# Optimization experiments

Hardware: AMD Instinct MI355X
Metric: run time of the kernel (lower is better)

## Reference

```python
import jax, jax.numpy as jnp
import numpy as np

B, S, D_MODEL = 2, 2048, 2048
N_HEADS, N_KV_HEADS, D_HEAD = 32, 8, 64
INIT_STD = 0.02


def setup_inputs() -> dict:
    key = jax.random.key(0)
    k1, k2, k3, k4, k5 = jax.random.split(key, 5)
    return {
        "residual": jax.random.normal(k1, (B, S, D_MODEL), dtype=jnp.float32),
        "W_Q": jax.random.normal(k2, (N_HEADS, D_HEAD, D_MODEL), dtype=jnp.float32) * INIT_STD,
        "W_K": jax.random.normal(k3, (N_KV_HEADS, D_HEAD, D_MODEL), dtype=jnp.float32) * INIT_STD,
        "W_V": jax.random.normal(k4, (N_KV_HEADS, D_HEAD, D_MODEL), dtype=jnp.float32) * INIT_STD,
        "W_O": jax.random.normal(k5, (N_HEADS, D_HEAD, D_MODEL), dtype=jnp.float32) * INIT_STD,
    }


def reference(residual, W_Q, W_K, W_V, W_O):
    # QKV projections: residual [b,p,d] x W [n,h,d] -> [b,p,n,h]
    q = jnp.einsum('bpd,nhd->bpnh', residual, W_Q)
    k = jnp.einsum('bpd,nhd->bpnh', residual, W_K)
    v = jnp.einsum('bpd,nhd->bpnh', residual, W_V)

    # GQA: repeat_interleave kv heads up to n_heads
    rep = N_HEADS // N_KV_HEADS
    k = jnp.repeat(k, rep, axis=2)  # [b, p, n_heads, h]
    v = jnp.repeat(v, rep, axis=2)

    # scaled dot-product scores: [b, n, q, k]
    scores = jnp.einsum('bqnh,bknh->bnqk', q, k) / jnp.sqrt(jnp.float32(D_HEAD))

    # causal mask (seq_len == total_len, no cache)
    seq_len = residual.shape[1]
    causal = jnp.tril(jnp.ones((seq_len, seq_len), dtype=bool))
    scores = jnp.where(causal[None, None, :, :], scores, jnp.float32(-jnp.inf))

    pattern = jax.nn.softmax(scores, axis=-1)

    # weighted sum of values: [b, q, n, h]
    attn_out = jnp.einsum('bnqk,bknh->bqnh', pattern, v)

    # output projection: [b, q, d_model]
    out = jnp.einsum('bqnh,nhd->bqd', attn_out, W_O)
    return out
```

## Files before the change

kernel.cpp:

```cpp
#include <hip/hip_runtime.h>


typedef __attribute__((ext_vector_type(8))) short short8;
typedef __attribute__((ext_vector_type(4))) short short4v;
typedef __attribute__((ext_vector_type(4))) float f32x4;

__device__ __forceinline__ short f2bs(float f) {
  unsigned u = __float_as_uint(f);
  u = (u + 0x7fffu + ((u >> 16) & 1u)) >> 16;
  return (short)u;
}
__device__ __forceinline__ float bs2f(short s) {
  return __uint_as_float(((unsigned)(unsigned short)s) << 16);
}

__device__ __forceinline__ void async_ld16(const void* g, void* l) {
  __builtin_amdgcn_global_load_lds((__attribute__((address_space(1))) void*)(g),
                                   (__attribute__((address_space(3))) void*)(l),
                                   16, 0, 0);
}

#define BARRIER()                       \
  do {                                  \
    asm volatile("" ::: "memory");      \
    __builtin_amdgcn_s_barrier();       \
    asm volatile("" ::: "memory");      \
  } while (0)
#define LGKM0()                                          \
  do {                                                   \
    asm volatile("s_waitcnt lgkmcnt(0)" ::: "memory");   \
    __builtin_amdgcn_sched_barrier(0);                   \
  } while (0)
#define VMCNT(n) asm volatile("s_waitcnt vmcnt(" #n ")" ::: "memory")
#define MFMA16(a, b, c) \
  (c) = __builtin_amdgcn_mfma_f32_16x16x32_bf16((a), (b), (c), 0, 0, 0)

__device__ __forceinline__ short4v pk4bf16(float p0, float p1, float p2,
                                           float p3) {
  union {
    unsigned u[2];
    short4v s;
  } pk;
  asm("v_cvt_pk_bf16_f32 %0, %1, %2" : "=v"(pk.u[0]) : "v"(p0), "v"(p1));
  asm("v_cvt_pk_bf16_f32 %0, %1, %2" : "=v"(pk.u[1]) : "v"(p2), "v"(p3));
  return pk.s;
}

__device__ __forceinline__ int block_sniff_f32(const short* __restrict__ r,
                                               int* bad) {
  if (threadIdx.x == 0) *bad = 0;
  __syncthreads();
  int my = 0;
  for (int i = threadIdx.x; i < 512; i += blockDim.x) {
    float x = bs2f(r[i]);
    if (!(fabsf(x) < 100.0f)) my = 1;
  }
  if (my) atomicOr(bad, 1);
  __syncthreads();
  return *bad;
}

__global__ __launch_bounds__(256) void prep_kernel(
    const void* __restrict__ s0, const void* __restrict__ s1,
    const void* __restrict__ s2, const void* __restrict__ s3,
    short* __restrict__ d0, short* __restrict__ d1, short* __restrict__ d2,
    short* __restrict__ d3, const void* __restrict__ wo,
    short* __restrict__ wot) {
  __shared__ short tile[64][65];
  __shared__ int badsh;
  const int isf = block_sniff_f32((const short*)s0, &badsh);
  const int bid = blockIdx.x;
  if (bid < 7168) {
    long off = (long)bid * 256 + threadIdx.x;
    const void* src;
    short* dst;
    if (off < 1048576) {
      src = s0; dst = d0;
    } else if ((off -= 1048576) < 524288) {
      src = s1; dst = d1;
    } else if ((off -= 524288) < 131072) {
      src = s2; dst = d2;
    } else {
      off -= 131072; src = s3; dst = d3;
    }
    const long e = off * 8;
    short8 v;
    if (isf) {
      const float* f = (const float*)src + e;
      const f32x4 a = *(const f32x4*)(f);
      const f32x4 b = *(const f32x4*)(f + 4);
#pragma unroll
      for (int j = 0; j < 4; ++j) {
        v[j] = f2bs(a[j]);
        v[4 + j] = f2bs(b[j]);
      }
    } else {
      v = *(const short8*)((const short*)src + e);
    }
    *(short8*)(dst + e) = v;
  } else {
    const int tb = bid - 7168;
    const int bx = tb & 31, by = tb >> 5;
    const int tx = threadIdx.x & 63, ty = threadIdx.x >> 6;
#pragma unroll
    for (int i = 0; i < 16; ++i) {
      const int r = ty + i * 4;
      const size_t idx = (size_t)(by * 64 + r) * 2048 + bx * 64 + tx;
      tile[r][tx] =
          isf ? f2bs(((const float*)wo)[idx]) : ((const short*)wo)[idx];
    }
    __syncthreads();
#pragma unroll
    for (int i = 0; i < 16; ++i) {
      const int r = ty + i * 4;
      wot[(size_t)(bx * 64 + r) * 2048 + by * 64 + tx] = tile[tx][r];
    }
  }
}

__device__ __forceinline__ void gemm256(const short* __restrict__ A, int lda,
                                        const short* __restrict__ B, int ldb,
                                        void* __restrict__ C, int ldc,
                                        int rowBase, int colBase, int K,
                                        short* SM, int outF32, float cscale) {
  const int t = threadIdx.x;
  const int wave = t >> 6;
  const int lane = t & 63;
  const int quad = lane >> 4;
  const int m16 = lane & 15;
  const int wr = (wave >> 2) * 128;
  const int wc = (wave & 3) * 64;

  short* const As0 = SM;
  short* const As1 = SM + 16384;
  short* const Bs0 = SM + 32768;
  short* const Bs1 = SM + 49152;

  const int sr = t >> 3;
  const int sc8 = ((t & 7) ^ (sr & 7)) * 8;
  const short* aS = A + (size_t)(rowBase + sr) * lda + sc8;
  const short* bS = B + (size_t)(colBase + sr) * ldb + sc8;
  const int dOff = wave * 512;

#define STG_A(buf, rg, kt) \
  async_ld16(aS + (size_t)(rg) * lda + (kt) * 64, (buf) + (rg) * 64 + dOff)
#define STG_B(buf, rg, kt) \
  async_ld16(bS + (size_t)(rg) * ldb + (kt) * 64, (buf) + (rg) * 64 + dOff)
#define RD(buf, row0, kh)                          \
  (*(const short8*)((buf) + ((row0) + m16) * 64 +  \
                    ((((kh) * 4 + quad) ^ (m16 & 7)) * 8)))

  const int nT = K >> 6;
  STG_A(As0, 0, 0); STG_A(As0, 64, 0); STG_A(As0, 128, 0); STG_A(As0, 192, 0);
  STG_B(Bs0, 0, 0); STG_B(Bs0, 64, 0); STG_B(Bs0, 128, 0); STG_B(Bs0, 192, 0);
  if (nT > 1) {
    STG_A(As1, 0, 1); STG_A(As1, 64, 1); STG_A(As1, 128, 1); STG_A(As1, 192, 1);
  }

  f32x4 acc[8][4] = {};
  for (int tt = 0; tt < nT; ++tt) {
    short* const Ac = (tt & 1) ? As1 : As0;
    short* const Bc = (tt & 1) ? Bs1 : Bs0;
    short* const Bn = (tt & 1) ? Bs0 : Bs1;

    if (tt + 1 < nT) {
      VMCNT(4);
    } else {
      VMCNT(0);
    }
    BARRIER();

    if (tt + 1 < nT) {
      STG_B(Bn, 0, tt + 1); STG_B(Bn, 64, tt + 1);
      STG_B(Bn, 128, tt + 1); STG_B(Bn, 192, tt + 1);
    }

    short8 alo[4][2], blo[2][2], bhi[2][2];
#pragma unroll
    for (int i = 0; i < 4; ++i) {
      alo[i][0] = RD(Ac, wr + i * 16, 0);
      alo[i][1] = RD(Ac, wr + i * 16, 1);
    }
#pragma unroll
    for (int j = 0; j < 2; ++j) {
      blo[j][0] = RD(Bc, wc + j * 16, 0);
      blo[j][1] = RD(Bc, wc + j * 16, 1);
    }
#pragma unroll
    for (int i = 0; i < 4; ++i)
#pragma unroll
      for (int j = 0; j < 2; ++j) {
        MFMA16(alo[i][0], blo[j][0], acc[i][j]);
        MFMA16(alo[i][1], blo[j][1], acc[i][j]);
      }
#pragma unroll
    for (int j = 0; j < 2; ++j) {
      bhi[j][0] = RD(Bc, wc + 32 + j * 16, 0);
      bhi[j][1] = RD(Bc, wc + 32 + j * 16, 1);
    }
#pragma unroll
    for (int i = 0; i < 4; ++i)
#pragma unroll
      for (int j = 0; j < 2; ++j) {
        MFMA16(alo[i][0], bhi[j][0], acc[i][2 + j]);
        MFMA16(alo[i][1], bhi[j][1], acc[i][2 + j]);
      }

    short8 ahi[4][2];
#pragma unroll
    for (int i = 0; i < 4; ++i) {
      ahi[i][0] = RD(Ac, wr + 64 + i * 16, 0);
      ahi[i][1] = RD(Ac, wr + 64 + i * 16, 1);
    }
    LGKM0();
    BARRIER();

    if (tt + 2 < nT) {
      STG_A(Ac, 0, tt + 2); STG_A(Ac, 64, tt + 2);
      STG_A(Ac, 128, tt + 2); STG_A(Ac, 192, tt + 2);
    }

#pragma unroll
    for (int i = 0; i < 4; ++i)
#pragma unroll
      for (int j = 0; j < 2; ++j) {
        MFMA16(ahi[i][0], blo[j][0], acc[4 + i][j]);
        MFMA16(ahi[i][1], blo[j][1], acc[4 + i][j]);
      }
#pragma unroll
    for (int i = 0; i < 4; ++i)
#pragma unroll
      for (int j = 0; j < 2; ++j) {
        MFMA16(ahi[i][0], bhi[j][0], acc[4 + i][2 + j]);
        MFMA16(ahi[i][1], bhi[j][1], acc[4 + i][2 + j]);
      }
  }

  float* const F = (float*)SM + wave * 4096;
#pragma unroll
  for (int h = 0; h < 2; ++h) {
    if (h) LGKM0();
#pragma unroll
    for (int i = 0; i < 4; ++i)
#pragma unroll
      for (int j = 0; j < 4; ++j)
#pragma unroll
        for (int r = 0; r < 4; ++r)
          F[(i * 16 + quad * 4 + r) * 64 + j * 16 + m16] =
              acc[h * 4 + i][j][r] * cscale;
    LGKM0();
#pragma unroll
    for (int p = 0; p < 16; ++p) {
      const int row = p * 4 + quad;
      const f32x4 vv = *(const f32x4*)(F + row * 64 + m16 * 4);
      const size_t gi =
          (size_t)(rowBase + wr + h * 64 + row) * ldc + colBase + wc + m16 * 4;
      if (outF32) {
        *(f32x4*)((float*)C + gi) = vv;
      } else {
        short4v s;
#pragma unroll
        for (int r = 0; r < 4; ++r) s[r] = f2bs(vv[r]);
        *(short4v*)((short*)C + gi) = s;
      }
    }
  }
#undef STG_A
#undef STG_B
#undef RD
}

__device__ __forceinline__ void gemm256x128(const short* __restrict__ A,
                                            int lda,
                                            const short* __restrict__ B,
                                            int ldb, void* __restrict__ C,
                                            int ldc, int rowBase, int colBase,
                                            int K, short* SM, int outF32) {
  const int t = threadIdx.x;
  const int wave = t >> 6;
  const int lane = t & 63;
  const int quad = lane >> 4;
  const int m16 = lane & 15;
  const int wr = (wave >> 1) * 64;
  const int wc = (wave & 1) * 64;

  short* const As0 = SM;
  short* const As1 = SM + 16384;
  short* const Bs0 = SM + 32768;
  short* const Bs1 = SM + 40960;

  const int sr = t >> 3;
  const int sc8 = ((t & 7) ^ (sr & 7)) * 8;
  const short* aS = A + (size_t)(rowBase + sr) * lda + sc8;
  const short* bS = B + (size_t)(colBase + sr) * ldb + sc8;
  const int dOff = wave * 512;

#define STG_A(buf, rg, kt) \
  async_ld16(aS + (size_t)(rg) * lda + (kt) * 64, (buf) + (rg) * 64 + dOff)
#define STG_B(buf, rg, kt) \
  async_ld16(bS + (size_t)(rg) * ldb + (kt) * 64, (buf) + (rg) * 64 + dOff)
#define RD(buf, row0, kh)                          \
  (*(const short8*)((buf) + ((row0) + m16) * 64 +  \
                    ((((kh) * 4 + quad) ^ (m16 & 7)) * 8)))

  const int nT = K >> 6;
  STG_A(As0, 0, 0); STG_A(As0, 64, 0); STG_A(As0, 128, 0); STG_A(As0, 192, 0);
  STG_B(Bs0, 0, 0); STG_B(Bs0, 64, 0);
  if (nT > 1) {
    STG_A(As1, 0, 1); STG_A(As1, 64, 1); STG_A(As1, 128, 1); STG_A(As1, 192, 1);
  }

  f32x4 acc[4][4] = {};
  for (int tt = 0; tt < nT; ++tt) {
    short* const Ac = (tt & 1) ? As1 : As0;
    short* const Bc = (tt & 1) ? Bs1 : Bs0;
    short* const Bn = (tt & 1) ? Bs0 : Bs1;

    if (tt + 1 < nT) {
      VMCNT(4);
    } else {
      VMCNT(0);
    }
    BARRIER();

    if (tt + 1 < nT) { STG_B(Bn, 0, tt + 1); STG_B(Bn, 64, tt + 1); }

    short8 a0[4], b0[4];
#pragma unroll
    for (int i = 0; i < 4; ++i) a0[i] = RD(Ac, wr + i * 16, 0);
#pragma unroll
    for (int j = 0; j < 4; ++j) b0[j] = RD(Bc, wc + j * 16, 0);
#pragma unroll
    for (int i = 0; i < 4; ++i)
#pragma unroll
      for (int j = 0; j < 4; ++j) MFMA16(a0[i], b0[j], acc[i][j]);

    short8 a1[4], b1[4];
#pragma unroll
    for (int i = 0; i < 4; ++i) a1[i] = RD(Ac, wr + i * 16, 1);
#pragma unroll
    for (int j = 0; j < 4; ++j) b1[j] = RD(Bc, wc + j * 16, 1);
    LGKM0();
    BARRIER();

    if (tt + 2 < nT) {
      STG_A(Ac, 0, tt + 2); STG_A(Ac, 64, tt + 2);
      STG_A(Ac, 128, tt + 2); STG_A(Ac, 192, tt + 2);
    }

#pragma unroll
    for (int i = 0; i < 4; ++i)
#pragma unroll
      for (int j = 0; j < 4; ++j) MFMA16(a1[i], b1[j], acc[i][j]);
  }

  float* const F = (float*)SM + wave * 4096;
#pragma unroll
  for (int i = 0; i < 4; ++i)
#pragma unroll
    for (int j = 0; j < 4; ++j)
#pragma unroll
      for (int r = 0; r < 4; ++r)
        F[(i * 16 + quad * 4 + r) * 64 + j * 16 + m16] = acc[i][j][r];
  LGKM0();
#pragma unroll
  for (int p = 0; p < 16; ++p) {
    const int row = p * 4 + quad;
    const f32x4 vv = *(const f32x4*)(F + row * 64 + m16 * 4);
    const size_t gi =
        (size_t)(rowBase + wr + row) * ldc + colBase + wc + m16 * 4;
    if (outF32) {
      *(f32x4*)((float*)C + gi) = vv;
    } else {
      short4v s;
#pragma unroll
      for (int r = 0; r < 4; ++r) s[r] = f2bs(vv[r]);
      *(short4v*)((short*)C + gi) = s;
    }
  }
#undef STG_A
#undef STG_B
#undef RD
}

__global__ __launch_bounds__(512, 2) void qkv_gemm_kernel(
    const short* __restrict__ R, const short* __restrict__ WQ,
    const short* __restrict__ WK, const short* __restrict__ WV,
    short* __restrict__ q, short* __restrict__ k, short* __restrict__ v) {
  __shared__ __align__(16) short SM[65536];
  const int lid = blockIdx.x;
  const int nl = (lid & 7) * 24 + (lid >> 3);
  const int ct = nl % 12;
  const int rt = nl / 12;
  const short* Bm;
  short* Cout;
  int colBase, ldc;
  float cs = 1.0f;
  if (ct < 8) {
    Bm = WQ; Cout = q; colBase = ct * 256; ldc = 2048;
    cs = 0.125f * 1.44269504088896340736f;
  } else if (ct < 10) {
    Bm = WK; Cout = k; colBase = (ct - 8) * 256; ldc = 512;
  } else {
    Bm = WV; Cout = v; colBase = (ct - 10) * 256; ldc = 512;
  }
  gemm256(R, 2048, Bm, 2048, Cout, ldc, rt * 256, colBase, 2048, SM, 0, cs);
}

__global__ __launch_bounds__(512, 2) void out_gemm_kernel(
    const short* __restrict__ A, const short* __restrict__ Bt,
    void* __restrict__ C, const short* __restrict__ sniffsrc) {
  __shared__ __align__(16) short SM[65536];
  const int outF32 = block_sniff_f32(sniffsrc, (int*)SM);
  const int lid = blockIdx.x;
  const int nl = (lid & 7) * 32 + (lid >> 3);
  const int ct = nl & 15;
  const int rt = nl >> 4;
  gemm256x128(A, 2048, Bt, 2048, C, 2048, rt * 256, ct * 128, 2048, SM,
              outF32);
}

__global__ __launch_bounds__(256) void vt_kernel(const short* __restrict__ v,
                                                 short* __restrict__ vt) {
  __shared__ short tile[64][65];
  const int hb = blockIdx.x * 64, pb = blockIdx.y * 64, b = blockIdx.z;
  const int tx = threadIdx.x & 63, ty = threadIdx.x >> 6;
#pragma unroll
  for (int i = 0; i < 16; ++i) {
    const int r = ty + i * 4;
    tile[r][tx] = v[((size_t)(b * 2048 + pb + r)) * 512 + hb + tx];
  }
  __syncthreads();
#pragma unroll
  for (int i = 0; i < 16; ++i) {
    const int r = ty + i * 4;
    vt[((size_t)(b * 512 + hb + r)) * 2048 + pb + tx] = tile[tx][r];
  }
}

__global__ __launch_bounds__(256, 3) void attn_kernel(
    const short* __restrict__ qbuf, const short* __restrict__ kbuf,
    const short* __restrict__ vtb, short* __restrict__ obuf) {
  __shared__ __align__(16) short Ks[2][64 * 64];
  __shared__ __align__(16) short Vs[2][64 * 64];
  __shared__ __align__(16) short Pb[4][32 * 64];

  const int b = blockIdx.x >> 3;
  const int kv = blockIdx.x & 7;
  const int qc = 63 - blockIdx.y;
  const int t = threadIdx.x;
  const int wave = t >> 6;
  const int hd = kv * 4 + wave;
  const int lane = t & 63;
  const int quad = lane >> 4;
  const int col = lane & 15;
  const int rb0 = qc * 32;

  short8 qf[2][2];
#pragma unroll
  for (int nt = 0; nt < 2; ++nt) {
    const int qr = rb0 + nt * 16 + col;
    const short* qp = qbuf + ((size_t)(b * 2048 + qr)) * 2048 + hd * 64 + quad * 8;
    qf[nt][0] = *(const short8*)(qp);
    qf[nt][1] = *(const short8*)(qp + 32);
  }

  short8 ones;
#pragma unroll
  for (int i = 0; i < 8; ++i) ones[i] = (short)0x3F80;

  f32x4 oacc[2][4] = {};
  f32x4 sacc[2] = {};

  short* P = &Pb[wave][0];
  const int swz = 4 * (col & 3);

  const int sRow = t >> 3;
  const int sPos = t & 7;
  const int r1 = sRow + 32;
  const short* kRow0 = kbuf + ((size_t)(b * 2048 + sRow)) * 512 + kv * 64 +
                       ((sPos ^ (sRow & 7)) * 8);
  const short* kRow1 = kbuf + ((size_t)(b * 2048 + r1)) * 512 + kv * 64 +
                       ((sPos ^ (r1 & 7)) * 8);
  const short* vRow0 = vtb + ((size_t)(b * 512 + kv * 64 + sRow)) * 2048 +
                       ((sPos ^ (sRow & 7)) * 8);
  const short* vRow1 = vtb + ((size_t)(b * 512 + kv * 64 + r1)) * 2048 +
                       ((sPos ^ (r1 & 7)) * 8);

  const int nkt = (qc >> 1) + 1;

  async_ld16(kRow0, &Ks[0][wave * 512]);
  async_ld16(kRow1, &Ks[0][2048 + wave * 512]);
  async_ld16(vRow0, &Vs[0][wave * 512]);
  async_ld16(vRow1, &Vs[0][2048 + wave * 512]);

  for (int kt = 0; kt < nkt; ++kt) {
    __syncthreads();
    if (kt + 1 < nkt) {
      const int nb = (kt + 1) & 1;
      const size_t ko = (size_t)(kt + 1) * 64 * 512;
      const int vo = (kt + 1) * 64;
      async_ld16(kRow0 + ko, &Ks[nb][wave * 512]);
      async_ld16(kRow1 + ko, &Ks[nb][2048 + wave * 512]);
      async_ld16(vRow0 + vo, &Vs[nb][wave * 512]);
      async_ld16(vRow1 + vo, &Vs[nb][2048 + wave * 512]);
    }
    const int ktb = kt * 64;
    const short* ks = &Ks[kt & 1][0];
    const short* vs = &Vs[kt & 1][0];

    short8 kf[4][2];
#pragma unroll
    for (int mt = 0; mt < 4; ++mt) {
      const int krow = mt * 16 + col;
      kf[mt][0] = *(const short8*)(ks + krow * 64 + ((quad ^ (col & 7)) * 8));
      kf[mt][1] = *(const short8*)(ks + krow * 64 + (((4 + quad) ^ (col & 7)) * 8));
    }

#pragma unroll
    for (int nt = 0; nt < 2; ++nt) {
      const int rb = rb0 + nt * 16;

      f32x4 st[4];
#pragma unroll
      for (int mt = 0; mt < 4; ++mt) {
        f32x4 z = {0.f, 0.f, 0.f, 0.f};
        z = __builtin_amdgcn_mfma_f32_16x16x32_bf16(kf[mt][0], qf[nt][0], z, 0, 0, 0);
        z = __builtin_amdgcn_mfma_f32_16x16x32_bf16(kf[mt][1], qf[nt][1], z, 0, 0, 0);
        st[mt] = z;
      }

      if (ktb + 63 > rb) {
        const int qrow = rb + col;
#pragma unroll
        for (int mt = 0; mt < 4; ++mt)
#pragma unroll
          for (int r = 0; r < 4; ++r)
            if (ktb + mt * 16 + quad * 4 + r > qrow) st[mt][r] = -1.0e30f;
      }

#pragma unroll
      for (int mt = 0; mt < 4; ++mt) {
        const float p0 = exp2f(st[mt][0]);
        const float p1 = exp2f(st[mt][1]);
        const float p2 = exp2f(st[mt][2]);
        const float p3 = exp2f(st[mt][3]);
        *(short4v*)(P + (nt * 16 + col) * 64 + (quad + 4 * (mt ^ (col & 3))) * 4) =
            pk4bf16(p0, p1, p2, p3);
      }
    }

    asm volatile("s_waitcnt lgkmcnt(0)" ::: "memory");

    short8 pf[2][2];
#pragma unroll
    for (int nt = 0; nt < 2; ++nt) {
      const int base = (nt * 16 + col) * 64;
      pf[nt][0] = *(const short8*)(P + base + ((2 * quad) ^ swz) * 4);
      pf[nt][1] = *(const short8*)(P + base + ((8 + 2 * quad) ^ swz) * 4);
    }

#pragma unroll
    for (int nt = 0; nt < 2; ++nt) {
      sacc[nt] = __builtin_amdgcn_mfma_f32_16x16x32_bf16(ones, pf[nt][0],
                                                         sacc[nt], 0, 0, 0);
      sacc[nt] = __builtin_amdgcn_mfma_f32_16x16x32_bf16(ones, pf[nt][1],
                                                         sacc[nt], 0, 0, 0);
    }

#pragma unroll
    for (int ct = 0; ct < 4; ++ct) {
      const int h = ct * 16 + col;
      const short8 va = *(const short8*)(vs + h * 64 + ((quad ^ (col & 7)) * 8));
      const short8 vb = *(const short8*)(vs + h * 64 + (((4 + quad) ^ (col & 7)) * 8));
#pragma unroll
      for (int nt = 0; nt < 2; ++nt) {
        oacc[nt][ct] = __builtin_amdgcn_mfma_f32_16x16x32_bf16(
            va, pf[nt][0], oacc[nt][ct], 0, 0, 0);
        oacc[nt][ct] = __builtin_amdgcn_mfma_f32_16x16x32_bf16(
            vb, pf[nt][1], oacc[nt][ct], 0, 0, 0);
      }
    }
  }

  const float inv0 = 1.0f / sacc[0][0];
  const float inv1 = 1.0f / sacc[1][0];
#pragma unroll
  for (int nt = 0; nt < 2; ++nt) {
    const float inv = nt ? inv1 : inv0;
#pragma unroll
    for (int ct = 0; ct < 4; ++ct) {
      *(short4v*)(P + (nt * 16 + col) * 64 + ct * 16 + quad * 4) =
          pk4bf16(oacc[nt][ct][0] * inv, oacc[nt][ct][1] * inv,
                  oacc[nt][ct][2] * inv, oacc[nt][ct][3] * inv);
    }
  }
  asm volatile("s_waitcnt lgkmcnt(0)" ::: "memory");
#pragma unroll
  for (int p = 0; p < 4; ++p) {
    const int qlocal = (lane >> 3) + 8 * p;
    const short8 row = *(const short8*)(P + qlocal * 64 + (lane & 7) * 8);
    *(short8*)(obuf + ((size_t)(b * 2048 + rb0 + qlocal)) * 2048 + hd * 64 +
               (lane & 7) * 8) = row;
  }
}

extern "C" void kernel_launch(void* const* d_in, const int* in_sizes, int n_in,
                              void* d_out, int out_size, void* d_ws,
                              size_t ws_size, hipStream_t stream) {
  char* ws = (char*)d_ws;
  short* rbuf = (short*)(ws + 256);
  short* wqb = rbuf + 8388608;
  short* wkb = wqb + 4194304;
  short* wvb = wkb + 1048576;
  short* kbuf = wvb + 1048576;
  short* vbuf = kbuf + 2097152;
  short* abuf = vbuf + 2097152;
  short* wot = abuf + 8388608;
  short* vtb = wqb;
  short* qbuf = (short*)d_out;

  hipLaunchKernelGGL(prep_kernel, dim3(8192), dim3(256), 0, stream,
                     d_in[0], d_in[1], d_in[2], d_in[3], rbuf, wqb, wkb, wvb,
                     d_in[4], wot);
  hipLaunchKernelGGL(qkv_gemm_kernel, dim3(192), dim3(512), 0, stream,
                     rbuf, wqb, wkb, wvb, qbuf, kbuf, vbuf);
  hipLaunchKernelGGL(vt_kernel, dim3(8, 32, 2), dim3(256), 0, stream,
                     vbuf, vtb);
  hipLaunchKernelGGL(attn_kernel, dim3(16, 64), dim3(256), 0, stream,
                     qbuf, kbuf, vtb, abuf);
  hipLaunchKernelGGL(out_gemm_kernel, dim3(256), dim3(512), 0, stream,
                     abuf, wot, (void*)d_out, (const short*)d_in[0]);
}
```

Before: 280.6 us.

## Fuse V transpose into QKV GEMM epilogue and raise MFMA priority in attention

The QKV GEMM now writes the V projection directly in transposed [b, kv*h, p] layout through its LDS staging epilogue, which removes the separate vt_kernel launch and its extra global read/write of V. The V-transposed buffer gets its own workspace slot instead of aliasing the W_Q buffer. Separately, the attention kernel wraps its MFMA sections in s_setprio to favor matrix-issue waves. The transposed epilogue reads LDS column-wise, which may cause bank conflicts and narrower global stores for the V tiles.

```diff
diff --git a/kernel.cpp b/kernel.cpp
--- a/kernel.cpp
+++ b/kernel.cpp
@@ -122,7 +122,8 @@
                                         const short* __restrict__ B, int ldb,
                                         void* __restrict__ C, int ldc,
                                         int rowBase, int colBase, int K,
-                                        short* SM, int outF32, float cscale) {
+                                        short* SM, int outF32, int outT,
+                                        float cscale) {
   const int t = threadIdx.x;
   const int wave = t >> 6;
   const int lane = t & 63;
@@ -249,19 +250,34 @@
           F[(i * 16 + quad * 4 + r) * 64 + j * 16 + m16] =
               acc[h * 4 + i][j][r] * cscale;
     LGKM0();
-#pragma unroll
-    for (int p = 0; p < 16; ++p) {
-      const int row = p * 4 + quad;
-      const f32x4 vv = *(const f32x4*)(F + row * 64 + m16 * 4);
-      const size_t gi =
-          (size_t)(rowBase + wr + h * 64 + row) * ldc + colBase + wc + m16 * 4;
-      if (outF32) {
-        *(f32x4*)((float*)C + gi) = vv;
-      } else {
+    if (outT) {
+      const int bb = rowBase >> 11;
+      const int pBase = (rowBase & 2047) + wr + h * 64;
+#pragma unroll
+      for (int p2 = 0; p2 < 16; ++p2) {
+        const int hl = p2 * 4 + quad;
         short4v s;
 #pragma unroll
-        for (int r = 0; r < 4; ++r) s[r] = f2bs(vv[r]);
-        *(short4v*)((short*)C + gi) = s;
+        for (int r = 0; r < 4; ++r) s[r] = f2bs(F[(m16 * 4 + r) * 64 + hl]);
+        *(short4v*)((short*)C +
+                    ((size_t)(bb * 512 + colBase + wc + hl)) * ldc + pBase +
+                    m16 * 4) = s;
+      }
+    } else {
+#pragma unroll
+      for (int p = 0; p < 16; ++p) {
+        const int row = p * 4 + quad;
+        const f32x4 vv = *(const f32x4*)(F + row * 64 + m16 * 4);
+        const size_t gi = (size_t)(rowBase + wr + h * 64 + row) * ldc +
+                          colBase + wc + m16 * 4;
+        if (outF32) {
+          *(f32x4*)((float*)C + gi) = vv;
+        } else {
+          short4v s;
+#pragma unroll
+          for (int r = 0; r < 4; ++r) s[r] = f2bs(vv[r]);
+          *(short4v*)((short*)C + gi) = s;
+        }
       }
     }
   }
@@ -386,7 +402,7 @@
 __global__ __launch_bounds__(512, 2) void qkv_gemm_kernel(
     const short* __restrict__ R, const short* __restrict__ WQ,
     const short* __restrict__ WK, const short* __restrict__ WV,
-    short* __restrict__ q, short* __restrict__ k, short* __restrict__ v) {
+    short* __restrict__ q, short* __restrict__ k, short* __restrict__ vtb) {
   __shared__ __align__(16) short SM[65536];
   const int lid = blockIdx.x;
   const int nl = (lid & 7) * 24 + (lid >> 3);
@@ -394,7 +410,7 @@
   const int rt = nl / 12;
   const short* Bm;
   short* Cout;
-  int colBase, ldc;
+  int colBase, ldc, outT = 0;
   float cs = 1.0f;
   if (ct < 8) {
     Bm = WQ; Cout = q; colBase = ct * 256; ldc = 2048;
@@ -402,9 +418,10 @@
   } else if (ct < 10) {
     Bm = WK; Cout = k; colBase = (ct - 8) * 256; ldc = 512;
   } else {
-    Bm = WV; Cout = v; colBase = (ct - 10) * 256; ldc = 512;
-  }
-  gemm256(R, 2048, Bm, 2048, Cout, ldc, rt * 256, colBase, 2048, SM, 0, cs);
+    Bm = WV; Cout = vtb; colBase = (ct - 10) * 256; ldc = 2048; outT = 1;
+  }
+  gemm256(R, 2048, Bm, 2048, Cout, ldc, rt * 256, colBase, 2048, SM, 0, outT,
+          cs);
 }
 
 __global__ __launch_bounds__(512, 2) void out_gemm_kernel(
@@ -420,24 +437,6 @@
               outF32);
 }
 
-__global__ __launch_bounds__(256) void vt_kernel(const short* __restrict__ v,
-                                                 short* __restrict__ vt) {
-  __shared__ short tile[64][65];
-  const int hb = blockIdx.x * 64, pb = blockIdx.y * 64, b = blockIdx.z;
-  const int tx = threadIdx.x & 63, ty = threadIdx.x >> 6;
-#pragma unroll
-  for (int i = 0; i < 16; ++i) {
-    const int r = ty + i * 4;
-    tile[r][tx] = v[((size_t)(b * 2048 + pb + r)) * 512 + hb + tx];
-  }
-  __syncthreads();
-#pragma unroll
-  for (int i = 0; i < 16; ++i) {
-    const int r = ty + i * 4;
-    vt[((size_t)(b * 512 + hb + r)) * 2048 + pb + tx] = tile[tx][r];
-  }
-}
-
 __global__ __launch_bounds__(256, 3) void attn_kernel(
     const short* __restrict__ qbuf, const short* __restrict__ kbuf,
     const short* __restrict__ vtb, short* __restrict__ obuf) {
@@ -522,6 +521,7 @@
       const int rb = rb0 + nt * 16;
 
       f32x4 st[4];
+      __builtin_amdgcn_s_setprio(1);
 #pragma unroll
       for (int mt = 0; mt < 4; ++mt) {
         f32x4 z = {0.f, 0.f, 0.f, 0.f};
@@ -529,6 +529,7 @@
         z = __builtin_amdgcn_mfma_f32_16x16x32_bf16(kf[mt][1], qf[nt][1], z, 0, 0, 0);
         st[mt] = z;
       }
+      __builtin_amdgcn_s_setprio(0);
 
       if (ktb + 63 > rb) {
         const int qrow = rb + col;
@@ -560,6 +561,7 @@
       pf[nt][1] = *(const short8*)(P + base + ((8 + 2 * quad) ^ swz) * 4);
     }
 
+    __builtin_amdgcn_s_setprio(1);
 #pragma unroll
     for (int nt = 0; nt < 2; ++nt) {
       sacc[nt] = __builtin_amdgcn_mfma_f32_16x16x32_bf16(ones, pf[nt][0],
@@ -581,6 +583,7 @@
             vb, pf[nt][1], oacc[nt][ct], 0, 0, 0);
       }
     }
+    __builtin_amdgcn_s_setprio(0);
   }
 
   const float inv0 = 1.0f / sacc[0][0];
@@ -614,19 +617,16 @@
   short* wkb = wqb + 4194304;
   short* wvb = wkb + 1048576;
   short* kbuf = wvb + 1048576;
-  short* vbuf = kbuf + 2097152;
-  short* abuf = vbuf + 2097152;
+  short* vtb = kbuf + 2097152;
+  short* abuf = vtb + 2097152;
   short* wot = abuf + 8388608;
-  short* vtb = wqb;
   short* qbuf = (short*)d_out;
 
   hipLaunchKernelGGL(prep_kernel, dim3(8192), dim3(256), 0, stream,
                      d_in[0], d_in[1], d_in[2], d_in[3], rbuf, wqb, wkb, wvb,
                      d_in[4], wot);
   hipLaunchKernelGGL(qkv_gemm_kernel, dim3(192), dim3(512), 0, stream,
-                     rbuf, wqb, wkb, wvb, qbuf, kbuf, vbuf);
-  hipLaunchKernelGGL(vt_kernel, dim3(8, 32, 2), dim3(256), 0, stream,
-                     vbuf, vtb);
+                     rbuf, wqb, wkb, wvb, qbuf, kbuf, vtb);
   hipLaunchKernelGGL(attn_kernel, dim3(16, 64), dim3(256), 0, stream,
                      qbuf, kbuf, vtb, abuf);
   hipLaunchKernelGGL(out_gemm_kernel, dim3(256), dim3(512), 0, stream,
```

New measurement: 289.9 us. 3.3% more time.
